# Performance work log

Measured on AMD Instinct MI355X. Metric: run time of the kernel, lower is better.

Reference implementation:

```python
import jax, jax.numpy as jnp
import numpy as np

NR, NS = 4, 3      # num_rotations, num_scales
RP, SP = 2, 2      # rotation_size, scale_size
K = 5              # kernel_size
PAD = 2
STRIDE = 1
NF = 9             # num basis functions (effective_size**2)


def setup_inputs() -> dict:
    key = jax.random.key(0)
    k1, k2, k3 = jax.random.split(key, 3)
    x = jax.random.normal(k1, (8, 16, NR * NS, 128, 128), dtype=jnp.float32)
    weight = jax.random.normal(k2, (16, 16, RP * SP, NF), dtype=jnp.float32) * 0.05
    basis = jax.random.normal(k3, (NF, NR * NS, K, K), dtype=jnp.float32)
    return {"x": x, "weight": weight, "basis": basis}


def reference(x, weight, basis):
    B, C, S, H, W = x.shape
    out_c, in_c, _, nf = weight.shape
    nrs = NR * NS
    # kernel synthesis: weight @ basis -> [nrs, out, in, RP*SP, K, K]
    kernel = jnp.einsum('oirf,fgxy->goirxy', weight, basis)
    kernel = kernel.reshape(nrs * out_c, in_c, RP, SP, K, K)
    # reshape input to [B, C, NR, NS, H, W]
    xg = x.reshape(B, C, NR, NS, H, W)
    # zero-pad scale axis at the end by SP-1
    xg = jnp.pad(xg, ((0, 0), (0, 0), (0, 0), (0, SP - 1), (0, 0), (0, 0)))
    # circular-pad rotation axis at the end by RP-1 (wrap from beginning)
    xg = jnp.concatenate([xg, xg[:, :, :RP - 1]], axis=2)
    out = None
    for i in range(RP):
        for j in range(SP):
            xs = xg[:, :, i:i + NR, j:j + NS]                     # [B,C,NR,NS,H,W]
            xs = xs.transpose(0, 2, 3, 1, 4, 5).reshape(B, nrs * C, H, W)
            o = jax.lax.conv_general_dilated(
                xs, kernel[:, :, i, j],
                window_strides=(STRIDE, STRIDE),
                padding=[(PAD, PAD), (PAD, PAD)],
                feature_group_count=nrs,
                dimension_numbers=('NCHW', 'OIHW', 'NCHW'))
            out = o if out is None else out + o
    B_, C_, H_, W_ = out.shape
    out = out.reshape(B_, nrs, out_c, H_, W_).transpose(0, 2, 1, 3, 4)
    return out
```

## Files before the change

kernel.cpp:

```cpp
#include <hip/hip_runtime.h>


#define NRS 12
#define CIN 16
#define COUT 16
#define HW 128
#define IMG (HW*HW)
#define ICSTRIDE (NRS*IMG)

#define HALO_H 36
#define HALO_W 20
#define ROWB 320
#define HALFB 11520
#define NCHUNK 1440
#define BUFB 24576
#define PADW 132
#define PADROWB (PADW*32)

typedef __bf16 bf16x8 __attribute__((ext_vector_type(8)));
typedef float  f32x4  __attribute__((ext_vector_type(4)));

__device__ __forceinline__ unsigned short f2bf(float f) {
    unsigned u = __builtin_bit_cast(unsigned, f);
    u += 0x7fffu + ((u >> 16) & 1u);
    return (unsigned short)(u >> 16);
}

__global__ void build_kc(const float* __restrict__ wgt, const float* __restrict__ basis,
                         unsigned short* __restrict__ kc) {
    int idx = blockIdx.x * 256 + threadIdx.x;
    const int total = 12 * 4 * 13 * 16 * 32;
    if (idx >= total) return;
    int k  = idx & 31;
    int possel = k >> 4, ic = k & 15;
    int o  = (idx >> 5) & 15;
    int t2 = idx >> 9;
    int pp = t2 % 13;
    int gr = t2 / 13;
    int rbase = gr & 3, g = gr >> 2;
    int pos = 2 * pp + possel;
    float s = 0.f;
    if (pos < 25) {
        int xk = pos / 5, yk = pos - 5 * xk;
        #pragma unroll
        for (int f = 0; f < 9; ++f)
            s = fmaf(wgt[((o * CIN + ic) * 4 + rbase) * 9 + f],
                     basis[((f * NRS + g) * 5 + xk) * 5 + yk], s);
    }
    kc[idx] = f2bf(s);
}

__global__ void cvt_pad(const float* __restrict__ x, unsigned short* __restrict__ xbf) {
    int idx = blockIdx.x * 256 + threadIdx.x;
    const int total = 8 * 12 * PADW * PADW;
    if (idx >= total) return;
    int wp = idx % PADW;
    int t1 = idx / PADW;
    int hp = t1 % PADW;
    int bs = t1 / PADW;
    int s  = bs % 12, bb = bs / 12;
    int h = hp - 2, w = wp - 2;
    bool ok = ((unsigned)h < 128u) && ((unsigned)w < 128u);
    const float* px = x + ((size_t)bb * 192 + s) * IMG + h * HW + w;
    unsigned short v[16];
    #pragma unroll
    for (int ic = 0; ic < 16; ++ic) {
        float f = 0.f;
        if (ok) f = px[(size_t)ic * ICSTRIDE];
        v[ic] = f2bf(f);
    }
    uint4 lo, hi;
    lo.x = v[0] | (v[1] << 16);  lo.y = v[2] | (v[3] << 16);
    lo.z = v[4] | (v[5] << 16);  lo.w = v[6] | (v[7] << 16);
    hi.x = v[8] | (v[9] << 16);  hi.y = v[10] | (v[11] << 16);
    hi.z = v[12] | (v[13] << 16); hi.w = v[14] | (v[15] << 16);
    *(uint4*)(xbf + (size_t)idx * 16)     = lo;
    *(uint4*)(xbf + (size_t)idx * 16 + 8) = hi;
}

__device__ __forceinline__ void stage_slice(const char* sb, char* lb, int wave, int lane) {
    #pragma unroll
    for (int j = 0; j < 6; ++j) {
        int c = wave * 384 + j * 64 + lane;
        int soff = 0;
        if (c < NCHUNK) {
            int hf = c / 720, p = c - hf * 720;
            int rl = p / 20, cl = p - rl * 20;
            soff = rl * PADROWB + cl * 32 + hf * 16;
        }
        __builtin_amdgcn_global_load_lds(
            (const __attribute__((address_space(1))) void*)(sb + soff),
            (__attribute__((address_space(3))) void*)(lb + j * 1024), 16, 0, 0);
    }
}

__global__ __launch_bounds__(256, 3)
void conv_fast(const unsigned short* __restrict__ xbf, const unsigned short* __restrict__ kc,
               float* __restrict__ out) {
    const int b   = blockIdx.z;
    const int r0  = blockIdx.y;
    const int th0 = (blockIdx.x >> 3) * 32;
    const int tw0 = (blockIdx.x & 7) * 16;

    const int t    = threadIdx.x;
    const int lane = t & 63;
    const int wave = t >> 6;
    const int n    = lane & 15;
    const int q    = lane >> 4;
    const int possel = q >> 1;
    const int half_  = q & 1;

    __shared__ uint4 xs4[(2 * BUFB) / 16];
    char* xsc = (char*)xs4;

    int boff[13];
    #pragma unroll
    for (int pp = 0; pp < 13; ++pp) {
        int pos = 2 * pp + possel; if (pos > 24) pos = 24;
        int dx = pos / 5, dy = pos - 5 * dx;
        boff[pp] = half_ * HALFB + dx * ROWB + (n + dy) * 16;
    }
    const int aoff = n * 32 + q * 8;

    f32x4 acc[3][8];
    #pragma unroll
    for (int s0 = 0; s0 < 3; ++s0)
        #pragma unroll
        for (int pg = 0; pg < 8; ++pg) acc[s0][pg] = (f32x4){0.f, 0.f, 0.f, 0.f};

    const char* xb0 = (const char*)xbf;
    const size_t tileoff = ((size_t)th0 * PADW + tw0) * 32;

    stage_slice(xb0 + ((size_t)(b * 12 + r0 * 3) * PADW * PADW) * 32 + tileoff,
                xsc + wave * 6144, wave, lane);
    __syncthreads();
    int cur = 0;

    #pragma unroll 1
    for (int i = 0; i < 2; ++i) {
        int rr = r0 + i; if (rr >= 4) rr -= 4;
        int rrn = rr + 1; if (rrn >= 4) rrn -= 4;
        #pragma unroll
        for (int ss = 0; ss < 3; ++ss) {
            if (i == 0 || ss < 2) {
                int sin_next = (ss < 2) ? (rr * 3 + ss + 1) : (rrn * 3);
                stage_slice(xb0 + ((size_t)(b * 12 + sin_next) * PADW * PADW) * 32 + tileoff,
                            xsc + (cur ^ 1) * BUFB + wave * 6144, wave, lane);
            }

            const unsigned short* kc0 = kc + (size_t)((r0 * 3 + ss) * 4 + 2 * i) * (13 * 512);
            const char* wb = xsc + cur * BUFB + wave * 8 * ROWB;
            if (ss > 0) {
                const unsigned short* kc1 = kc + (size_t)((r0 * 3 + ss - 1) * 4 + 2 * i + 1) * (13 * 512);
                #pragma unroll
                for (int pp = 0; pp < 13; ++pp) {
                    bf16x8 af0 = *(const bf16x8*)(kc0 + pp * 512 + aoff);
                    bf16x8 af1 = *(const bf16x8*)(kc1 + pp * 512 + aoff);
                    const char* wp = wb + boff[pp];
                    #pragma unroll
                    for (int pg = 0; pg < 8; ++pg) {
                        bf16x8 bfv = *(const bf16x8*)(wp + pg * ROWB);
                        acc[ss][pg]     = __builtin_amdgcn_mfma_f32_16x16x32_bf16(af0, bfv, acc[ss][pg], 0, 0, 0);
                        acc[ss - 1][pg] = __builtin_amdgcn_mfma_f32_16x16x32_bf16(af1, bfv, acc[ss - 1][pg], 0, 0, 0);
                    }
                }
            } else {
                #pragma unroll
                for (int pp = 0; pp < 13; ++pp) {
                    bf16x8 af0 = *(const bf16x8*)(kc0 + pp * 512 + aoff);
                    const char* wp = wb + boff[pp];
                    #pragma unroll
                    for (int pg = 0; pg < 8; ++pg) {
                        bf16x8 bfv = *(const bf16x8*)(wp + pg * ROWB);
                        acc[ss][pg] = __builtin_amdgcn_mfma_f32_16x16x32_bf16(af0, bfv, acc[ss][pg], 0, 0, 0);
                    }
                }
            }
            __syncthreads();
            cur ^= 1;
        }
    }

    #pragma unroll
    for (int s0 = 0; s0 < 3; ++s0) {
        const size_t obase = ((size_t)b * COUT * NRS + (r0 * 3 + s0)) * IMG;
        #pragma unroll
        for (int pg = 0; pg < 8; ++pg) {
            int row = th0 + wave * 8 + pg;
            int col = tw0 + n;
            size_t pix = (size_t)row * HW + col;
            #pragma unroll
            for (int r = 0; r < 4; ++r) {
                int o = q * 4 + r;
                out[obase + (size_t)o * NRS * IMG + pix] = acc[s0][pg][r];
            }
        }
    }
}

__global__ __launch_bounds__(256, 2)
void conv_slow(const float* __restrict__ x, const unsigned short* __restrict__ kc,
               float* __restrict__ out) {
    const int b   = blockIdx.z;
    const int r0  = blockIdx.y;
    const int th0 = (blockIdx.x >> 3) * 32;
    const int tw0 = (blockIdx.x & 7) * 16;

    const int t    = threadIdx.x;
    const int lane = t & 63;
    const int wave = t >> 6;
    const int n    = lane & 15;
    const int q    = lane >> 4;
    const int possel = q >> 1;
    const int half_  = q & 1;

    __shared__ uint4 xs4[(2 * HALFB) / 16];
    char* xsc = (char*)xs4;

    int boff[13];
    #pragma unroll
    for (int pp = 0; pp < 13; ++pp) {
        int pos = 2 * pp + possel; if (pos > 24) pos = 24;
        int dx = pos / 5, dy = pos - 5 * dx;
        boff[pp] = half_ * HALFB + dx * ROWB + (n + dy) * 16;
    }
    const int aoff = n * 32 + q * 8;

    f32x4 acc[3][8];
    #pragma unroll
    for (int s0 = 0; s0 < 3; ++s0)
        #pragma unroll
        for (int pg = 0; pg < 8; ++pg) acc[s0][pg] = (f32x4){0.f, 0.f, 0.f, 0.f};

    #pragma unroll 1
    for (int i = 0; i < 2; ++i) {
        int rr = r0 + i; if (rr >= 4) rr -= 4;
        #pragma unroll
        for (int ss = 0; ss < 3; ++ss) {
            const int sin_ = rr * 3 + ss;
            const float* xb = x + ((size_t)b * CIN * NRS + sin_) * IMG;

            __syncthreads();
            for (int p = t; p < 720; p += 256) {
                int rl = p / HALO_W, cl = p - rl * HALO_W;
                int hh = th0 + rl - 2, ww = tw0 + cl - 2;
                bool ok = ((unsigned)hh < 128u) && ((unsigned)ww < 128u);
                const float* px = xb + hh * HW + ww;
                unsigned short v[16];
                #pragma unroll
                for (int ic = 0; ic < 16; ++ic) {
                    float f = 0.f;
                    if (ok) f = px[(size_t)ic * ICSTRIDE];
                    v[ic] = f2bf(f);
                }
                uint4 lo, hi;
                lo.x = v[0] | (v[1] << 16);  lo.y = v[2] | (v[3] << 16);
                lo.z = v[4] | (v[5] << 16);  lo.w = v[6] | (v[7] << 16);
                hi.x = v[8] | (v[9] << 16);  hi.y = v[10] | (v[11] << 16);
                hi.z = v[12] | (v[13] << 16); hi.w = v[14] | (v[15] << 16);
                *(uint4*)(xsc + p * 16)         = lo;
                *(uint4*)(xsc + HALFB + p * 16) = hi;
            }
            __syncthreads();

            const unsigned short* kc0 = kc + (size_t)((r0 * 3 + ss) * 4 + 2 * i) * (13 * 512);
            const unsigned short* kc1 = kc + (size_t)((r0 * 3 + ss - 1) * 4 + 2 * i + 1) * (13 * 512);
            const char* wb = xsc + wave * 8 * ROWB;
            #pragma unroll
            for (int pp = 0; pp < 13; ++pp) {
                bf16x8 af0 = *(const bf16x8*)(kc0 + pp * 512 + aoff);
                bf16x8 af1;
                if (ss > 0) af1 = *(const bf16x8*)(kc1 + pp * 512 + aoff);
                const char* wp = wb + boff[pp];
                #pragma unroll
                for (int pg = 0; pg < 8; ++pg) {
                    bf16x8 bfv = *(const bf16x8*)(wp + pg * ROWB);
                    acc[ss][pg] = __builtin_amdgcn_mfma_f32_16x16x32_bf16(af0, bfv, acc[ss][pg], 0, 0, 0);
                    if (ss > 0)
                        acc[ss - 1][pg] = __builtin_amdgcn_mfma_f32_16x16x32_bf16(af1, bfv, acc[ss - 1][pg], 0, 0, 0);
                }
            }
        }
    }

    #pragma unroll
    for (int s0 = 0; s0 < 3; ++s0) {
        const size_t obase = ((size_t)b * COUT * NRS + (r0 * 3 + s0)) * IMG;
        #pragma unroll
        for (int pg = 0; pg < 8; ++pg) {
            int row = th0 + wave * 8 + pg;
            int col = tw0 + n;
            size_t pix = (size_t)row * HW + col;
            #pragma unroll
            for (int r = 0; r < 4; ++r) {
                int o = q * 4 + r;
                out[obase + (size_t)o * NRS * IMG + pix] = acc[s0][pg][r];
            }
        }
    }
}

extern "C" void kernel_launch(void* const* d_in, const int* in_sizes, int n_in,
                              void* d_out, int out_size, void* d_ws, size_t ws_size,
                              hipStream_t stream) {
    const float* x      = (const float*)d_in[0];
    const float* weight = (const float*)d_in[1];
    const float* basis  = (const float*)d_in[2];
    float* out = (float*)d_out;
    unsigned short* kc = (unsigned short*)d_ws;

    build_kc<<<dim3((12 * 4 * 13 * 16 * 32 + 255) / 256), dim3(256), 0, stream>>>(weight, basis, kc);

    const size_t xbf_off = 655360;
    const size_t xbf_bytes = (size_t)8 * 12 * PADW * PADW * 32;
    if (ws_size >= xbf_off + xbf_bytes) {
        unsigned short* xbf = (unsigned short*)((char*)d_ws + xbf_off);
        cvt_pad<<<dim3((8 * 12 * PADW * PADW + 255) / 256), dim3(256), 0, stream>>>(x, xbf);
        conv_fast<<<dim3(32, 4, 8), dim3(256), 0, stream>>>(xbf, kc, out);
    } else {
        conv_slow<<<dim3(32, 4, 8), dim3(256), 0, stream>>>(x, kc, out);
    }
}
```

Measured before the change: 279.5 us.

## Give each wave private LDS halo buffers and replace block barriers with vmcnt waits

Each wave now stages its own 12-row halo (8 output rows plus 4 halo rows) into a private double buffer, using global_load_lds. It then waits on its own loads with s_waitcnt vmcnt instead of block-wide __syncthreads. This removes inter-wave barrier stalls, so waves can run independently and overlap their loads with MFMA work. In exchange, the overlapping halo rows are loaded redundantly across waves and LDS use grows to 64KB per block, so occupancy drops to 2 blocks per CU.

```diff
diff --git a/kernel.cpp b/kernel.cpp
--- a/kernel.cpp
+++ b/kernel.cpp
@@ -8,12 +8,11 @@
 #define IMG (HW*HW)
 #define ICSTRIDE (NRS*IMG)
 
-#define HALO_H 36
 #define HALO_W 20
 #define ROWB 320
-#define HALFB 11520
-#define NCHUNK 1440
-#define BUFB 24576
+#define WHALFB 3840
+#define WCHUNK 480
+#define WBUF 8192
 #define PADW 132
 #define PADROWB (PADW*32)
 
@@ -78,23 +77,20 @@
     *(uint4*)(xbf + (size_t)idx * 16 + 8) = hi;
 }
 
-__device__ __forceinline__ void stage_slice(const char* sb, char* lb, int wave, int lane) {
-    #pragma unroll
-    for (int j = 0; j < 6; ++j) {
-        int c = wave * 384 + j * 64 + lane;
-        int soff = 0;
-        if (c < NCHUNK) {
-            int hf = c / 720, p = c - hf * 720;
-            int rl = p / 20, cl = p - rl * 20;
-            soff = rl * PADROWB + cl * 32 + hf * 16;
-        }
+__device__ __forceinline__ void stage_wave(const char* sb, char* lb, int lane) {
+    #pragma unroll
+    for (int j = 0; j < 8; ++j) {
+        int c = j * 64 + lane; if (c > WCHUNK - 1) c = WCHUNK - 1;
+        int hf = c / 240, p = c - hf * 240;
+        int rl = p / 20, cl = p - rl * 20;
+        int soff = rl * PADROWB + cl * 32 + hf * 16;
         __builtin_amdgcn_global_load_lds(
             (const __attribute__((address_space(1))) void*)(sb + soff),
             (__attribute__((address_space(3))) void*)(lb + j * 1024), 16, 0, 0);
     }
 }
 
-__global__ __launch_bounds__(256, 3)
+__global__ __launch_bounds__(256, 2)
 void conv_fast(const unsigned short* __restrict__ xbf, const unsigned short* __restrict__ kc,
                float* __restrict__ out) {
     const int b   = blockIdx.z;
@@ -110,15 +106,16 @@
     const int possel = q >> 1;
     const int half_  = q & 1;
 
-    __shared__ uint4 xs4[(2 * BUFB) / 16];
+    __shared__ uint4 xs4[65536 / 16];
     char* xsc = (char*)xs4;
+    char* mybase = xsc + wave * (2 * WBUF);
 
     int boff[13];
     #pragma unroll
     for (int pp = 0; pp < 13; ++pp) {
         int pos = 2 * pp + possel; if (pos > 24) pos = 24;
         int dx = pos / 5, dy = pos - 5 * dx;
-        boff[pp] = half_ * HALFB + dx * ROWB + (n + dy) * 16;
+        boff[pp] = half_ * WHALFB + dx * ROWB + (n + dy) * 16;
     }
     const int aoff = n * 32 + q * 8;
 
@@ -129,13 +126,11 @@
         for (int pg = 0; pg < 8; ++pg) acc[s0][pg] = (f32x4){0.f, 0.f, 0.f, 0.f};
 
     const char* xb0 = (const char*)xbf;
-    const size_t tileoff = ((size_t)th0 * PADW + tw0) * 32;
-
-    stage_slice(xb0 + ((size_t)(b * 12 + r0 * 3) * PADW * PADW) * 32 + tileoff,
-                xsc + wave * 6144, wave, lane);
-    __syncthreads();
+    const size_t waveoff = ((size_t)(th0 + wave * 8) * PADW + tw0) * 32;
+
+    stage_wave(xb0 + ((size_t)(b * 12 + r0 * 3) * PADW * PADW) * 32 + waveoff, mybase, lane);
+
     int cur = 0;
-
     #pragma unroll 1
     for (int i = 0; i < 2; ++i) {
         int rr = r0 + i; if (rr >= 4) rr -= 4;
@@ -144,12 +139,15 @@
         for (int ss = 0; ss < 3; ++ss) {
             if (i == 0 || ss < 2) {
                 int sin_next = (ss < 2) ? (rr * 3 + ss + 1) : (rrn * 3);
-                stage_slice(xb0 + ((size_t)(b * 12 + sin_next) * PADW * PADW) * 32 + tileoff,
-                            xsc + (cur ^ 1) * BUFB + wave * 6144, wave, lane);
+                stage_wave(xb0 + ((size_t)(b * 12 + sin_next) * PADW * PADW) * 32 + waveoff,
+                           mybase + (cur ^ 1) * WBUF, lane);
+                asm volatile("s_waitcnt vmcnt(8)" ::: "memory");
+            } else {
+                asm volatile("s_waitcnt vmcnt(0)" ::: "memory");
             }
 
             const unsigned short* kc0 = kc + (size_t)((r0 * 3 + ss) * 4 + 2 * i) * (13 * 512);
-            const char* wb = xsc + cur * BUFB + wave * 8 * ROWB;
+            const char* wb = mybase + cur * WBUF;
             if (ss > 0) {
                 const unsigned short* kc1 = kc + (size_t)((r0 * 3 + ss - 1) * 4 + 2 * i + 1) * (13 * 512);
                 #pragma unroll
@@ -176,7 +174,6 @@
                     }
                 }
             }
-            __syncthreads();
             cur ^= 1;
         }
     }
@@ -214,7 +211,7 @@
     const int possel = q >> 1;
     const int half_  = q & 1;
 
-    __shared__ uint4 xs4[(2 * HALFB) / 16];
+    __shared__ uint4 xs4[(2 * 11520) / 16];
     char* xsc = (char*)xs4;
 
     int boff[13];
@@ -222,7 +219,7 @@
     for (int pp = 0; pp < 13; ++pp) {
         int pos = 2 * pp + possel; if (pos > 24) pos = 24;
         int dx = pos / 5, dy = pos - 5 * dx;
-        boff[pp] = half_ * HALFB + dx * ROWB + (n + dy) * 16;
+        boff[pp] = half_ * 11520 + dx * 320 + (n + dy) * 16;
     }
     const int aoff = n * 32 + q * 8;
 
@@ -259,13 +256,13 @@
                 hi.x = v[8] | (v[9] << 16);  hi.y = v[10] | (v[11] << 16);
                 hi.z = v[12] | (v[13] << 16); hi.w = v[14] | (v[15] << 16);
                 *(uint4*)(xsc + p * 16)         = lo;
-                *(uint4*)(xsc + HALFB + p * 16) = hi;
+                *(uint4*)(xsc + 11520 + p * 16) = hi;
             }
             __syncthreads();
 
             const unsigned short* kc0 = kc + (size_t)((r0 * 3 + ss) * 4 + 2 * i) * (13 * 512);
             const unsigned short* kc1 = kc + (size_t)((r0 * 3 + ss - 1) * 4 + 2 * i + 1) * (13 * 512);
-            const char* wb = xsc + wave * 8 * ROWB;
+            const char* wb = xsc + wave * 8 * 320;
             #pragma unroll
             for (int pp = 0; pp < 13; ++pp) {
                 bf16x8 af0 = *(const bf16x8*)(kc0 + pp * 512 + aoff);
@@ -274,7 +271,7 @@
                 const char* wp = wb + boff[pp];
                 #pragma unroll
                 for (int pg = 0; pg < 8; ++pg) {
-                    bf16x8 bfv = *(const bf16x8*)(wp + pg * ROWB);
+                    bf16x8 bfv = *(const bf16x8*)(wp + pg * 320);
                     acc[ss][pg] = __builtin_amdgcn_mfma_f32_16x16x32_bf16(af0, bfv, acc[ss][pg], 0, 0, 0);
                     if (ss > 0)
                         acc[ss - 1][pg] = __builtin_amdgcn_mfma_f32_16x16x32_bf16(af1, bfv, acc[ss - 1][pg], 0, 0, 0);
```

Measured after the change: 253.2 us. 9.4% less time.
